# Performance work log

Measured on AMD Instinct MI355X. Metric: run time of the kernel, lower is better.

## Reference

```python
import jax, jax.numpy as jnp
import numpy as np

B, S, D, H = 2, 2048, 2048, 16
HD = D // H  # 128 head dim


def setup_inputs() -> dict:
    key = jax.random.key(0)
    k1, k2, k3 = jax.random.split(key, 3)
    x = jax.random.normal(k1, (B, S, D), dtype=jnp.float32)
    w_qkv = jax.random.normal(k2, (3 * D, D), dtype=jnp.float32) * 0.02
    w_out = jax.random.normal(k3, (D, D), dtype=jnp.float32) * 0.02
    # complex-like RoPE table: freqs_cis[s, j] = exp(i * s * theta^{-2j/hd})
    theta = 10000.0
    inv_freq = 1.0 / (theta ** (jnp.arange(0, HD, 2, dtype=jnp.float32) / HD))  # [HD/2]
    t = jnp.arange(S, dtype=jnp.float32)
    freqs = jnp.outer(t, inv_freq)  # [S, HD/2]
    return {"x": x, "w_qkv": w_qkv, "w_out": w_out,
            "freqs_cos": jnp.cos(freqs), "freqs_sin": jnp.sin(freqs)}


def _apply_rope(t, cos, sin):
    # t: [b, s, h, hd]; adjacent pairs treated as complex (real, imag)
    b, s, h, hd = t.shape
    tr = t.reshape(b, s, h, hd // 2, 2)
    re, im = tr[..., 0], tr[..., 1]
    c = cos[None, :, None, :]  # [1, s, 1, hd/2]
    sn = sin[None, :, None, :]
    out_re = re * c - im * sn
    out_im = re * sn + im * c
    return jnp.stack([out_re, out_im], axis=-1).reshape(b, s, h, hd)


def reference(x, w_qkv, w_out, freqs_cos, freqs_sin):
    b, s, d = x.shape
    qkv = x @ w_qkv.T  # [b, s, 3d]
    q, k, v = jnp.split(qkv, 3, axis=-1)
    q = q.reshape(b, s, H, HD)
    k = k.reshape(b, s, H, HD)
    v = v.reshape(b, s, H, HD)
    q = _apply_rope(q, freqs_cos, freqs_sin)
    k = _apply_rope(k, freqs_cos, freqs_sin)
    # causal SDPA
    scale = 1.0 / jnp.sqrt(jnp.asarray(HD, dtype=x.dtype))
    scores = jnp.einsum("bqhd,bkhd->bhqk", q, k) * scale  # [b, h, s, s]
    causal = jnp.tril(jnp.ones((s, s), dtype=bool))
    scores = jnp.where(causal[None, None], scores, jnp.finfo(scores.dtype).min)
    attn = jax.nn.softmax(scores, axis=-1)
    out = jnp.einsum("bhqk,bkhd->bqhd", attn, v).reshape(b, s, d)
    return out @ w_out.T
```

## Files before the change

### kernel.cpp

```cpp
#include <hip/hip_runtime.h>
#include <hip/hip_bf16.h>
#include <stdint.h>

#define S_ 2048
#define D_ 2048
#define H_ 16
#define HD_ 128

typedef __bf16 bf16x8 __attribute__((ext_vector_type(8)));
typedef float f32x4 __attribute__((ext_vector_type(4)));
typedef unsigned short ushort_t;
typedef ushort_t us4 __attribute__((ext_vector_type(4)));

__device__ __forceinline__ float bf2f(ushort_t u) {
  union { float f; uint32_t i; } x; x.i = ((uint32_t)u) << 16; return x.f;
}
__device__ __forceinline__ ushort_t f2bf(float f) {
  union { float f; uint32_t i; } x; x.f = f;
  uint32_t r = x.i + 0x7fffu + ((x.i >> 16) & 1u);
  return (ushort_t)(r >> 16);
}

__device__ __forceinline__ void async_copy16(const void* g, void* l) {
  __builtin_amdgcn_global_load_lds(
      (const __attribute__((address_space(1))) unsigned int*)g,
      (__attribute__((address_space(3))) unsigned int*)l, 16, 0, 0);
}

__device__ __forceinline__ void store_val(float* p, float v) { *p = v; }
__device__ __forceinline__ void store_val(ushort_t* p, float v) { *p = f2bf(v); }

__global__ __launch_bounds__(256) void cvt_f32_bf16(const float* __restrict__ in,
                                                    ushort_t* __restrict__ out,
                                                    int n4) {
  int i = blockIdx.x * 256 + threadIdx.x;
  if (i >= n4) return;
  const float4 v = ((const float4*)in)[i];
  us4 o;
  o.x = f2bf(v.x); o.y = f2bf(v.y); o.z = f2bf(v.z); o.w = f2bf(v.w);
  ((us4*)out)[i] = o;
}

template <typename OutT>
__global__ __launch_bounds__(256) void gemm_bt(const ushort_t* __restrict__ A,
                                               const ushort_t* __restrict__ Bm,
                                               OutT* __restrict__ C,
                                               int M, int N, int K) {
  __shared__ __align__(16) ushort_t As[128 * 32];
  __shared__ __align__(16) ushort_t Bs[128 * 32];
  const int tid = threadIdx.x;
  const int wave = tid >> 6, lane = tid & 63;
  const int quad = lane >> 4, l16 = lane & 15;
  const int bm = blockIdx.y * 128, bn = blockIdx.x * 128;
  const int wm = (wave >> 1) * 64, wn = (wave & 1) * 64;

  f32x4 acc[4][4] = {};

  const int c0 = wave * 2, c1 = c0 + 1;
  const int srow = lane >> 2;
  const int scol = (lane & 3) * 8;
  const ushort_t* gA0 = A + (size_t)(bm + c0 * 16 + srow) * K + scol;
  const ushort_t* gA1 = A + (size_t)(bm + c1 * 16 + srow) * K + scol;
  const ushort_t* gB0 = Bm + (size_t)(bn + c0 * 16 + srow) * K + scol;
  const ushort_t* gB1 = Bm + (size_t)(bn + c1 * 16 + srow) * K + scol;
  ushort_t* lA0 = As + c0 * 512;
  ushort_t* lA1 = As + c1 * 512;
  ushort_t* lB0 = Bs + c0 * 512;
  ushort_t* lB1 = Bs + c1 * 512;

  for (int k0 = 0; k0 < K; k0 += 32) {
    __syncthreads();
    async_copy16(gA0 + k0, lA0);
    async_copy16(gA1 + k0, lA1);
    async_copy16(gB0 + k0, lB0);
    async_copy16(gB1 + k0, lB1);
    __syncthreads();
    bf16x8 af[4], bfr[4];
#pragma unroll
    for (int i = 0; i < 4; ++i)
      af[i] = *(const bf16x8*)(As + (wm + i * 16 + l16) * 32 + quad * 8);
#pragma unroll
    for (int i = 0; i < 4; ++i)
      bfr[i] = *(const bf16x8*)(Bs + (wn + i * 16 + l16) * 32 + quad * 8);
#pragma unroll
    for (int mi = 0; mi < 4; ++mi)
#pragma unroll
      for (int ni = 0; ni < 4; ++ni)
        acc[mi][ni] = __builtin_amdgcn_mfma_f32_16x16x32_bf16(af[mi], bfr[ni],
                                                              acc[mi][ni], 0, 0, 0);
  }
#pragma unroll
  for (int mi = 0; mi < 4; ++mi)
#pragma unroll
    for (int ni = 0; ni < 4; ++ni)
#pragma unroll
      for (int r = 0; r < 4; ++r) {
        int row = bm + wm + mi * 16 + quad * 4 + r;
        int col = bn + wn + ni * 16 + l16;
        store_val(&C[(size_t)row * N + col], acc[mi][ni][r]);
      }
}

__device__ __forceinline__ void stage_half(const ushort_t* __restrict__ g, int K,
                                           ushort_t* l, int wave, int srow,
                                           int clog) {
#pragma unroll
  for (int i = 0; i < 2; ++i)
    async_copy16(g + (size_t)(i * 64 + srow) * K + clog * 8,
                 l + wave * 512 + i * 4096);
}

#define MFMA_BF16(a, b, c) __builtin_amdgcn_mfma_f32_16x16x32_bf16(a, b, c, 0, 0, 0)

template <typename OutT>
__global__ __launch_bounds__(512, 2) void gemm_bt256(const ushort_t* __restrict__ A,
                                                     const ushort_t* __restrict__ Bm,
                                                     OutT* __restrict__ C,
                                                     int M, int N, int K) {
  __shared__ __align__(16) ushort_t As[2][256 * 64];
  __shared__ __align__(16) ushort_t Bs[2][256 * 64];
  const int tid = threadIdx.x;
  const int wave = tid >> 6, lane = tid & 63;
  const int quad = lane >> 4, l16 = lane & 15;
  const int bm = blockIdx.y * 256, bn = blockIdx.x * 256;
  const int wm = (wave >> 2) * 128;
  const int wn = (wave & 3) * 64;
  const int srow = tid >> 3;
  const int clog = (tid & 7) ^ (srow & 7);
  const int ck0 = (quad ^ (l16 & 7)) * 8;
  const int ck1 = ((4 + quad) ^ (l16 & 7)) * 8;

  const ushort_t* gA = A + (size_t)bm * K;
  const ushort_t* gB = Bm + (size_t)bn * K;
  const int NT = K >> 6;

  f32x4 acc[8][4] = {};

  stage_half(gA, K, &As[0][0], wave, srow, clog);
  stage_half(gA + (size_t)128 * K, K, &As[0][8192], wave, srow, clog);
  stage_half(gB, K, &Bs[0][0], wave, srow, clog);
  stage_half(gB + (size_t)128 * K, K, &Bs[0][8192], wave, srow, clog);
  if (NT > 1) {
    stage_half(gA + 64, K, &As[1][0], wave, srow, clog);
    stage_half(gA + (size_t)128 * K + 64, K, &As[1][8192], wave, srow, clog);
    stage_half(gB + 64, K, &Bs[1][0], wave, srow, clog);
    stage_half(gB + (size_t)128 * K + 64, K, &Bs[1][8192], wave, srow, clog);
    asm volatile("s_waitcnt vmcnt(8)" ::: "memory");
  } else {
    asm volatile("s_waitcnt vmcnt(0)" ::: "memory");
  }
  __builtin_amdgcn_sched_barrier(0);
  __builtin_amdgcn_s_barrier();

  for (int t = 0; t < NT; ++t) {
    ushort_t* A_cur = &As[t & 1][0];
    ushort_t* B_cur = &Bs[t & 1][0];
    const ushort_t* Arow = A_cur + (wm + l16) * 64;
    const ushort_t* Brow = B_cur + (wn + l16) * 64;
    const size_t kn2 = (size_t)(t + 2) * 64;
    const bool pf2 = (t + 2 < NT);

    bf16x8 a4[4][2], b01[2][2], b23[2][2];

#pragma unroll
    for (int mi = 0; mi < 4; ++mi) {
      a4[mi][0] = *(const bf16x8*)(Arow + mi * 1024 + ck0);
      a4[mi][1] = *(const bf16x8*)(Arow + mi * 1024 + ck1);
    }
#pragma unroll
    for (int ni = 0; ni < 2; ++ni) {
      b01[ni][0] = *(const bf16x8*)(Brow + ni * 1024 + ck0);
      b01[ni][1] = *(const bf16x8*)(Brow + ni * 1024 + ck1);
    }
    __builtin_amdgcn_s_barrier();
    __builtin_amdgcn_s_setprio(1);
#pragma unroll
    for (int ks = 0; ks < 2; ++ks)
#pragma unroll
      for (int mi = 0; mi < 4; ++mi)
#pragma unroll
        for (int ni = 0; ni < 2; ++ni)
          acc[mi][ni] = MFMA_BF16(a4[mi][ks], b01[ni][ks], acc[mi][ni]);
    __builtin_amdgcn_s_setprio(0);
    __builtin_amdgcn_s_barrier();

#pragma unroll
    for (int ni = 0; ni < 2; ++ni) {
      b23[ni][0] = *(const bf16x8*)(Brow + (ni + 2) * 1024 + ck0);
      b23[ni][1] = *(const bf16x8*)(Brow + (ni + 2) * 1024 + ck1);
    }
    __builtin_amdgcn_s_barrier();
    __builtin_amdgcn_s_setprio(1);
#pragma unroll
    for (int ks = 0; ks < 2; ++ks)
#pragma unroll
      for (int mi = 0; mi < 4; ++mi)
#pragma unroll
        for (int ni = 0; ni < 2; ++ni)
          acc[mi][ni + 2] = MFMA_BF16(a4[mi][ks], b23[ni][ks], acc[mi][ni + 2]);
    __builtin_amdgcn_s_setprio(0);
    __builtin_amdgcn_s_barrier();

#pragma unroll
    for (int mi = 0; mi < 4; ++mi) {
      a4[mi][0] = *(const bf16x8*)(Arow + (mi + 4) * 1024 + ck0);
      a4[mi][1] = *(const bf16x8*)(Arow + (mi + 4) * 1024 + ck1);
    }
    if (pf2) {
      stage_half(gB + kn2, K, B_cur, wave, srow, clog);
      stage_half(gB + (size_t)128 * K + kn2, K, B_cur + 8192, wave, srow, clog);
    }
    __builtin_amdgcn_s_barrier();
    __builtin_amdgcn_s_setprio(1);
#pragma unroll
    for (int ks = 0; ks < 2; ++ks)
#pragma unroll
      for (int mi = 0; mi < 4; ++mi)
#pragma unroll
        for (int ni = 0; ni < 2; ++ni)
          acc[mi + 4][ni] = MFMA_BF16(a4[mi][ks], b01[ni][ks], acc[mi + 4][ni]);
    __builtin_amdgcn_s_setprio(0);
    __builtin_amdgcn_s_barrier();

    if (pf2) {
      stage_half(gA + kn2, K, A_cur, wave, srow, clog);
      stage_half(gA + (size_t)128 * K + kn2, K, A_cur + 8192, wave, srow, clog);
      asm volatile("s_waitcnt vmcnt(8)" ::: "memory");
    } else {
      asm volatile("s_waitcnt vmcnt(0)" ::: "memory");
    }
    __builtin_amdgcn_sched_barrier(0);
    __builtin_amdgcn_s_barrier();
    __builtin_amdgcn_s_setprio(1);
#pragma unroll
    for (int ks = 0; ks < 2; ++ks)
#pragma unroll
      for (int mi = 0; mi < 4; ++mi)
#pragma unroll
        for (int ni = 0; ni < 2; ++ni)
          acc[mi + 4][ni + 2] = MFMA_BF16(a4[mi][ks], b23[ni][ks], acc[mi + 4][ni + 2]);
    __builtin_amdgcn_s_setprio(0);
    __builtin_amdgcn_s_barrier();
    __builtin_amdgcn_sched_barrier(0);
  }

#pragma unroll
  for (int mi = 0; mi < 8; ++mi)
#pragma unroll
    for (int ni = 0; ni < 4; ++ni)
#pragma unroll
      for (int r = 0; r < 4; ++r) {
        int row = bm + wm + mi * 16 + quad * 4 + r;
        int col = bn + wn + ni * 16 + l16;
        store_val(&C[(size_t)row * N + col], acc[mi][ni][r]);
      }
}

__global__ __launch_bounds__(256) void rope_k(ushort_t* __restrict__ qkv,
                                              const float* __restrict__ fc,
                                              const float* __restrict__ fs) {
  int idx = blockIdx.x * 256 + threadIdx.x;
  int i = idx & 63;
  int hh = (idx >> 6) & 15;
  int m = idx >> 10;
  int s = m & (S_ - 1);
  float c = fc[s * 64 + i], sn = fs[s * 64 + i];
  size_t off = (size_t)m * (3 * D_) + hh * HD_ + 2 * i;
#pragma unroll
  for (int part = 0; part < 2; ++part) {
    uint32_t* p = (uint32_t*)(qkv + off + part * D_);
    uint32_t v = *p;
    float re = bf2f((ushort_t)(v & 0xffffu));
    float im = bf2f((ushort_t)(v >> 16));
    float nr = re * c - im * sn;
    float ni = re * sn + im * c;
    *p = (uint32_t)f2bf(nr) | ((uint32_t)f2bf(ni) << 16);
  }
}

__global__ __launch_bounds__(256) void vt_prep(const ushort_t* __restrict__ qkv,
                                               ushort_t* __restrict__ VTg) {
  __shared__ __align__(16) ushort_t T[64 * 136];
  const int st = blockIdx.x, h = blockIdx.y, b = blockIdx.z;
  const int tid = threadIdx.x;
  const ushort_t* gV = qkv + (size_t)(b * S_ + st * 64) * (3 * D_) + 2 * D_ + h * HD_;
  {
    const int r = tid >> 2, cc = (tid & 3) * 32;
    const ushort_t* src = gV + (size_t)r * (3 * D_) + cc;
    uint4 a0 = ((const uint4*)src)[0];
    uint4 a1 = ((const uint4*)src)[1];
    uint4 a2 = ((const uint4*)src)[2];
    uint4 a3 = ((const uint4*)src)[3];
    ushort_t* dst = T + r * 136 + cc;
    ((uint4*)dst)[0] = a0; ((uint4*)dst)[1] = a1;
    ((uint4*)dst)[2] = a2; ((uint4*)dst)[3] = a3;
  }
  __syncthreads();
  const int d = tid >> 1, kh = (tid & 1) * 32;
  ushort_t buf[32];
#pragma unroll
  for (int j = 0; j < 32; ++j) buf[j] = T[(kh + j) * 136 + d];
  ushort_t* out = VTg + ((size_t)((b * H_ + h) * HD_ + d)) * S_ + st * 64 + kh;
  ((uint4*)out)[0] = *(const uint4*)(buf + 0);
  ((uint4*)out)[1] = *(const uint4*)(buf + 8);
  ((uint4*)out)[2] = *(const uint4*)(buf + 16);
  ((uint4*)out)[3] = *(const uint4*)(buf + 24);
}

#define SOFTMAX_C 12.0f

__global__ __launch_bounds__(256, 4) void attn_fwd(const ushort_t* __restrict__ qkv,
                                                   const ushort_t* __restrict__ VTg,
                                                   float* __restrict__ Oacc,
                                                   float* __restrict__ lsum_g) {
  __shared__ __align__(16) ushort_t Kl[64 * 128];
  __shared__ __align__(16) ushort_t VT[128 * 64];
  __shared__ __align__(16) ushort_t Pl[4 * 16 * 64];

  const int j = 79 - (int)blockIdx.x;
  int qt, c;
  if (j < 8)       { qt = j;                 c = 0; }
  else if (j < 24) { int t = j - 8;  qt = 8 + (t >> 1);  c = t & 1; }
  else if (j < 48) { int t = j - 24; qt = 16 + t / 3;    c = t % 3; }
  else             { int t = j - 48; qt = 24 + (t >> 2); c = t & 3; }
  const int h = blockIdx.y, b = blockIdx.z;
  const int kt0 = c * 8;
  const int kt_end = min(kt0 + 8, qt + 1);

  const int tid = threadIdx.x;
  const int wave = tid >> 6, lane = tid & 63;
  const int quad = lane >> 4, l16 = lane & 15;
  const float scale = 0.08838834764831845f;

  const int qg = qt * 64 + wave * 16 + l16;
  const ushort_t* qrow = qkv + (size_t)(b * S_ + qg) * (3 * D_) + h * HD_;
  bf16x8 qf[4];
#pragma unroll
  for (int cc = 0; cc < 4; ++cc)
    qf[cc] = *(const bf16x8*)(qrow + cc * 32 + quad * 8);

  f32x4 o[8] = {};
  float lsum[4] = {0.f, 0.f, 0.f, 0.f};
  const int q_row_base = qt * 64 + wave * 16 + quad * 4;
  ushort_t* Pw = Pl + wave * 16 * 64;

  const ushort_t* gK = qkv + (size_t)(b * S_) * (3 * D_) + D_ + h * HD_;
  const ushort_t* gVT = VTg + (size_t)(b * H_ + h) * HD_ * S_;

  const int krow_off = lane >> 4;
  const int kchunk = lane & 15;
  const int vrow_off = lane >> 3;
  const int vchunk = lane & 7;

  for (int kt = kt0; kt < kt_end; ++kt) {
    __syncthreads();
#pragma unroll
    for (int i = 0; i < 4; ++i) {
      int row = wave * 16 + i * 4 + krow_off;
      int lchunk = kchunk ^ (row & 15);
      async_copy16(gK + (size_t)(kt * 64 + row) * (3 * D_) + lchunk * 8,
                   Kl + (wave * 16 + i * 4) * 128);
    }
#pragma unroll
    for (int i = 0; i < 4; ++i) {
      int row = wave * 32 + i * 8 + vrow_off;
      int lchunk = vchunk ^ (row & 7);
      async_copy16(gVT + (size_t)row * S_ + kt * 64 + lchunk * 8,
                   VT + (wave * 32 + i * 8) * 64);
    }
    __syncthreads();

    const bool diag = (kt == qt);
#pragma unroll
    for (int g = 0; g < 4; ++g) {
      f32x4 s = {0.f, 0.f, 0.f, 0.f};
#pragma unroll
      for (int cc = 0; cc < 4; ++cc) {
        bf16x8 kf = *(const bf16x8*)(Kl + (g * 16 + l16) * 128 +
                                     (((cc * 4 + quad) ^ l16) * 8));
        s = __builtin_amdgcn_mfma_f32_16x16x32_bf16(qf[cc], kf, s, 0, 0, 0);
      }
      const int key = kt * 64 + g * 16 + l16;
#pragma unroll
      for (int r = 0; r < 4; ++r) {
        float e = __expf(s[r] * scale - SOFTMAX_C);
        float p = (!diag || key <= q_row_base + r) ? e : 0.f;
        lsum[r] += p;
        int prow = quad * 4 + r;
        int pcol = g * 16 + l16;
        Pw[prow * 64 + (((pcol >> 3) ^ (prow & 7)) * 8) + (pcol & 7)] = f2bf(p);
      }
    }
    bf16x8 pf0 = *(const bf16x8*)(Pw + l16 * 64 + ((quad ^ (l16 & 7)) * 8));
    bf16x8 pf1 = *(const bf16x8*)(Pw + l16 * 64 + (((4 + quad) ^ (l16 & 7)) * 8));
#pragma unroll
    for (int dc = 0; dc < 8; ++dc) {
      bf16x8 v0 = *(const bf16x8*)(VT + (dc * 16 + l16) * 64 +
                                   (((0 * 4 + quad) ^ (l16 & 7)) * 8));
      o[dc] = __builtin_amdgcn_mfma_f32_16x16x32_bf16(pf0, v0, o[dc], 0, 0, 0);
      bf16x8 v1 = *(const bf16x8*)(VT + (dc * 16 + l16) * 64 +
                                   (((1 * 4 + quad) ^ (l16 & 7)) * 8));
      o[dc] = __builtin_amdgcn_mfma_f32_16x16x32_bf16(pf1, v1, o[dc], 0, 0, 0);
    }
  }

#pragma unroll
  for (int r = 0; r < 4; ++r) {
    float l = lsum[r];
    l += __shfl_xor(l, 1, 64);
    l += __shfl_xor(l, 2, 64);
    l += __shfl_xor(l, 4, 64);
    l += __shfl_xor(l, 8, 64);
    size_t row = (size_t)(b * S_ + q_row_base + r);
    if (l16 == 0) unsafeAtomicAdd(&lsum_g[row * H_ + h], l);
#pragma unroll
    for (int dc = 0; dc < 8; ++dc)
      unsafeAtomicAdd(&Oacc[row * D_ + h * HD_ + dc * 16 + l16], o[dc][r]);
  }
}

__global__ __launch_bounds__(256) void combine(const float* __restrict__ Oacc,
                                               const float* __restrict__ lsum_g,
                                               ushort_t* __restrict__ attn) {
  int i = blockIdx.x * 256 + threadIdx.x;
  float4 v = ((const float4*)Oacc)[i];
  int flat = i * 4;
  int row = flat >> 11;
  int h = (flat >> 7) & 15;
  float inv = 1.0f / lsum_g[row * H_ + h];
  us4 o;
  o.x = f2bf(v.x * inv); o.y = f2bf(v.y * inv);
  o.z = f2bf(v.z * inv); o.w = f2bf(v.w * inv);
  ((us4*)attn)[i] = o;
}

extern "C" void kernel_launch(void* const* d_in, const int* in_sizes, int n_in,
                              void* d_out, int out_size, void* d_ws, size_t ws_size,
                              hipStream_t stream) {
  const float* x = (const float*)d_in[0];
  const float* w_qkv = (const float*)d_in[1];
  const float* w_out = (const float*)d_in[2];
  const float* fcos = (const float*)d_in[3];
  const float* fsin = (const float*)d_in[4];
  float* out = (float*)d_out;

  char* ws = (char*)d_ws;
  ushort_t* x_bf    = (ushort_t*)(ws + 0);
  ushort_t* wqkv_bf = (ushort_t*)(ws + 16777216);
  ushort_t* wout_bf = (ushort_t*)(ws + 41943040);
  ushort_t* qkv     = (ushort_t*)(ws + 50331648);
  ushort_t* attn    = (ushort_t*)(ws + 100663296);
  float* Oacc   = (float*)(ws + 0);
  float* lsum_g = (float*)(ws + 33554432);
  ushort_t* VTg = (ushort_t*)(ws + 100663296);

  cvt_f32_bf16<<<8192, 256, 0, stream>>>(x, x_bf, 2097152);
  cvt_f32_bf16<<<12288, 256, 0, stream>>>(w_qkv, wqkv_bf, 3145728);
  cvt_f32_bf16<<<4096, 256, 0, stream>>>(w_out, wout_bf, 1048576);

  gemm_bt256<ushort_t><<<dim3(24, 16), 512, 0, stream>>>(x_bf, wqkv_bf, qkv,
                                                         4096, 6144, 2048);
  rope_k<<<16384, 256, 0, stream>>>(qkv, fcos, fsin);
  vt_prep<<<dim3(32, 16, 2), 256, 0, stream>>>(qkv, VTg);

  hipMemsetAsync(Oacc, 0, 33554432, stream);
  hipMemsetAsync(lsum_g, 0, 262144, stream);

  attn_fwd<<<dim3(80, 16, 2), 256, 0, stream>>>(qkv, VTg, Oacc, lsum_g);
  combine<<<8192, 256, 0, stream>>>(Oacc, lsum_g, attn);

  gemm_bt<float><<<dim3(16, 32), 256, 0, stream>>>(attn, wout_bf, out,
                                                   4096, 2048, 2048);
}
```

Before: 460.9 us.

## Restructure GEMM main loop into unrolled ping-pong with staggered A/B prefetch

Unrolls the GEMM K-loop by two so LDS buffer pointers are fixed even/odd constants, and spreads the global-to-LDS prefetches of A and B half-tiles across the four MFMA phases instead of batching them. A is now loaded only one tile ahead while B stays two ahead, with a uniform vmcnt(4) wait. The intent is to smooth memory traffic, cut per-iteration address arithmetic and branches, and overlap loads with MFMA better. It assumes an even tile count and clamps prefetch indices at the tail, which issues some redundant loads.

```diff
diff --git a/kernel.cpp b/kernel.cpp
--- a/kernel.cpp
+++ b/kernel.cpp
@@ -136,42 +136,42 @@
 
   f32x4 acc[8][4] = {};
 
+  const ushort_t* ArowE = &As[0][0] + (wm + l16) * 64;
+  const ushort_t* BrowE = &Bs[0][0] + (wn + l16) * 64;
+  const ushort_t* ArowO = &As[1][0] + (wm + l16) * 64;
+  const ushort_t* BrowO = &Bs[1][0] + (wn + l16) * 64;
+
+  stage_half(gB, K, &Bs[0][0], wave, srow, clog);
+  stage_half(gB + (size_t)128 * K, K, &Bs[0][8192], wave, srow, clog);
   stage_half(gA, K, &As[0][0], wave, srow, clog);
   stage_half(gA + (size_t)128 * K, K, &As[0][8192], wave, srow, clog);
-  stage_half(gB, K, &Bs[0][0], wave, srow, clog);
-  stage_half(gB + (size_t)128 * K, K, &Bs[0][8192], wave, srow, clog);
-  if (NT > 1) {
-    stage_half(gA + 64, K, &As[1][0], wave, srow, clog);
-    stage_half(gA + (size_t)128 * K + 64, K, &As[1][8192], wave, srow, clog);
-    stage_half(gB + 64, K, &Bs[1][0], wave, srow, clog);
-    stage_half(gB + (size_t)128 * K + 64, K, &Bs[1][8192], wave, srow, clog);
-    asm volatile("s_waitcnt vmcnt(8)" ::: "memory");
-  } else {
-    asm volatile("s_waitcnt vmcnt(0)" ::: "memory");
-  }
+  stage_half(gB + 64, K, &Bs[1][0], wave, srow, clog);
+  stage_half(gB + (size_t)128 * K + 64, K, &Bs[1][8192], wave, srow, clog);
+  asm volatile("s_waitcnt vmcnt(4)" ::: "memory");
   __builtin_amdgcn_sched_barrier(0);
   __builtin_amdgcn_s_barrier();
 
-  for (int t = 0; t < NT; ++t) {
-    ushort_t* A_cur = &As[t & 1][0];
-    ushort_t* B_cur = &Bs[t & 1][0];
-    const ushort_t* Arow = A_cur + (wm + l16) * 64;
-    const ushort_t* Brow = B_cur + (wn + l16) * 64;
-    const size_t kn2 = (size_t)(t + 2) * 64;
-    const bool pf2 = (t + 2 < NT);
+  for (int ii = 0; ii < (NT >> 1); ++ii) {
+    const int t = 2 * ii;
+    const int t2 = (t + 2 < NT) ? t + 2 : NT - 1;
+    const int t3 = (t + 3 < NT) ? t + 3 : NT - 1;
+    const size_t k1 = (size_t)(t + 1) * 64;
+    const size_t k2 = (size_t)t2 * 64;
+    const size_t k3 = (size_t)t3 * 64;
 
     bf16x8 a4[4][2], b01[2][2], b23[2][2];
 
 #pragma unroll
     for (int mi = 0; mi < 4; ++mi) {
-      a4[mi][0] = *(const bf16x8*)(Arow + mi * 1024 + ck0);
-      a4[mi][1] = *(const bf16x8*)(Arow + mi * 1024 + ck1);
+      a4[mi][0] = *(const bf16x8*)(ArowE + mi * 1024 + ck0);
+      a4[mi][1] = *(const bf16x8*)(ArowE + mi * 1024 + ck1);
     }
 #pragma unroll
     for (int ni = 0; ni < 2; ++ni) {
-      b01[ni][0] = *(const bf16x8*)(Brow + ni * 1024 + ck0);
-      b01[ni][1] = *(const bf16x8*)(Brow + ni * 1024 + ck1);
-    }
+      b01[ni][0] = *(const bf16x8*)(BrowE + ni * 1024 + ck0);
+      b01[ni][1] = *(const bf16x8*)(BrowE + ni * 1024 + ck1);
+    }
+    stage_half(gA + k1, K, &As[1][0], wave, srow, clog);
     __builtin_amdgcn_s_barrier();
     __builtin_amdgcn_s_setprio(1);
 #pragma unroll
@@ -186,9 +186,10 @@
 
 #pragma unroll
     for (int ni = 0; ni < 2; ++ni) {
-      b23[ni][0] = *(const bf16x8*)(Brow + (ni + 2) * 1024 + ck0);
-      b23[ni][1] = *(const bf16x8*)(Brow + (ni + 2) * 1024 + ck1);
-    }
+      b23[ni][0] = *(const bf16x8*)(BrowE + (ni + 2) * 1024 + ck0);
+      b23[ni][1] = *(const bf16x8*)(BrowE + (ni + 2) * 1024 + ck1);
+    }
+    stage_half(gA + (size_t)128 * K + k1, K, &As[1][8192], wave, srow, clog);
     __builtin_amdgcn_s_barrier();
     __builtin_amdgcn_s_setprio(1);
 #pragma unroll
@@ -203,13 +204,10 @@
 
 #pragma unroll
     for (int mi = 0; mi < 4; ++mi) {
-      a4[mi][0] = *(const bf16x8*)(Arow + (mi + 4) * 1024 + ck0);
-      a4[mi][1] = *(const bf16x8*)(Arow + (mi + 4) * 1024 + ck1);
-    }
-    if (pf2) {
-      stage_half(gB + kn2, K, B_cur, wave, srow, clog);
-      stage_half(gB + (size_t)128 * K + kn2, K, B_cur + 8192, wave, srow, clog);
-    }
+      a4[mi][0] = *(const bf16x8*)(ArowE + (mi + 4) * 1024 + ck0);
+      a4[mi][1] = *(const bf16x8*)(ArowE + (mi + 4) * 1024 + ck1);
+    }
+    stage_half(gB + k2, K, &Bs[0][0], wave, srow, clog);
     __builtin_amdgcn_s_barrier();
     __builtin_amdgcn_s_setprio(1);
 #pragma unroll
@@ -222,13 +220,82 @@
     __builtin_amdgcn_s_setprio(0);
     __builtin_amdgcn_s_barrier();
 
-    if (pf2) {
-      stage_half(gA + kn2, K, A_cur, wave, srow, clog);
-      stage_half(gA + (size_t)128 * K + kn2, K, A_cur + 8192, wave, srow, clog);
-      asm volatile("s_waitcnt vmcnt(8)" ::: "memory");
-    } else {
-      asm volatile("s_waitcnt vmcnt(0)" ::: "memory");
-    }
+    stage_half(gB + (size_t)128 * K + k2, K, &Bs[0][8192], wave, srow, clog);
+    asm volatile("s_waitcnt vmcnt(4)" ::: "memory");
+    __builtin_amdgcn_sched_barrier(0);
+    __builtin_amdgcn_s_barrier();
+    __builtin_amdgcn_s_setprio(1);
+#pragma unroll
+    for (int ks = 0; ks < 2; ++ks)
+#pragma unroll
+      for (int mi = 0; mi < 4; ++mi)
+#pragma unroll
+        for (int ni = 0; ni < 2; ++ni)
+          acc[mi + 4][ni + 2] = MFMA_BF16(a4[mi][ks], b23[ni][ks], acc[mi + 4][ni + 2]);
+    __builtin_amdgcn_s_setprio(0);
+    __builtin_amdgcn_s_barrier();
+
+#pragma unroll
+    for (int mi = 0; mi < 4; ++mi) {
+      a4[mi][0] = *(const bf16x8*)(ArowO + mi * 1024 + ck0);
+      a4[mi][1] = *(const bf16x8*)(ArowO + mi * 1024 + ck1);
+    }
+#pragma unroll
+    for (int ni = 0; ni < 2; ++ni) {
+      b01[ni][0] = *(const bf16x8*)(BrowO + ni * 1024 + ck0);
+      b01[ni][1] = *(const bf16x8*)(BrowO + ni * 1024 + ck1);
+    }
+    stage_half(gA + k2, K, &As[0][0], wave, srow, clog);
+    __builtin_amdgcn_s_barrier();
+    __builtin_amdgcn_s_setprio(1);
+#pragma unroll
+    for (int ks = 0; ks < 2; ++ks)
+#pragma unroll
+      for (int mi = 0; mi < 4; ++mi)
+#pragma unroll
+        for (int ni = 0; ni < 2; ++ni)
+          acc[mi][ni] = MFMA_BF16(a4[mi][ks], b01[ni][ks], acc[mi][ni]);
+    __builtin_amdgcn_s_setprio(0);
+    __builtin_amdgcn_s_barrier();
+
+#pragma unroll
+    for (int ni = 0; ni < 2; ++ni) {
+      b23[ni][0] = *(const bf16x8*)(BrowO + (ni + 2) * 1024 + ck0);
+      b23[ni][1] = *(const bf16x8*)(BrowO + (ni + 2) * 1024 + ck1);
+    }
+    stage_half(gA + (size_t)128 * K + k2, K, &As[0][8192], wave, srow, clog);
+    __builtin_amdgcn_s_barrier();
+    __builtin_amdgcn_s_setprio(1);
+#pragma unroll
+    for (int ks = 0; ks < 2; ++ks)
+#pragma unroll
+      for (int mi = 0; mi < 4; ++mi)
+#pragma unroll
+        for (int ni = 0; ni < 2; ++ni)
+          acc[mi][ni + 2] = MFMA_BF16(a4[mi][ks], b23[ni][ks], acc[mi][ni + 2]);
+    __builtin_amdgcn_s_setprio(0);
+    __builtin_amdgcn_s_barrier();
+
+#pragma unroll
+    for (int mi = 0; mi < 4; ++mi) {
+      a4[mi][0] = *(const bf16x8*)(ArowO + (mi + 4) * 1024 + ck0);
+      a4[mi][1] = *(const bf16x8*)(ArowO + (mi + 4) * 1024 + ck1);
+    }
+    stage_half(gB + k3, K, &Bs[1][0], wave, srow, clog);
+    __builtin_amdgcn_s_barrier();
+    __builtin_amdgcn_s_setprio(1);
+#pragma unroll
+    for (int ks = 0; ks < 2; ++ks)
+#pragma unroll
+      for (int mi = 0; mi < 4; ++mi)
+#pragma unroll
+        for (int ni = 0; ni < 2; ++ni)
+          acc[mi + 4][ni] = MFMA_BF16(a4[mi][ks], b01[ni][ks], acc[mi + 4][ni]);
+    __builtin_amdgcn_s_setprio(0);
+    __builtin_amdgcn_s_barrier();
+
+    stage_half(gB + (size_t)128 * K + k3, K, &Bs[1][8192], wave, srow, clog);
+    asm volatile("s_waitcnt vmcnt(4)" ::: "memory");
     __builtin_amdgcn_sched_barrier(0);
     __builtin_amdgcn_s_barrier();
     __builtin_amdgcn_s_setprio(1);
@@ -243,6 +310,8 @@
     __builtin_amdgcn_s_barrier();
     __builtin_amdgcn_sched_barrier(0);
   }
+
+  asm volatile("s_waitcnt vmcnt(0)" ::: "memory");
 
 #pragma unroll
   for (int mi = 0; mi < 8; ++mi)
```

New measurement: 452.9 us. About the same (-1.7%).
